# Optimization experiments

Measured on AMD Instinct MI355X. Metric: run time of the kernel, lower is better.

## Reference

```python
import jax, jax.numpy as jnp
import numpy as np

B, T, V, D, OUT = 32, 100, 10000, 128, 1000
CODE_P = 0.003  # ~30 active codes per visit


def gru_dir(x3, whh, bhh, reverse):
    """x3: [B,T,3F] precomputed input-side gates (W_ih x + b_ih). PyTorch GRU math."""
    F = whh.shape[1]
    h0 = jnp.zeros((x3.shape[0], F), x3.dtype)

    def step(h, xt):
        gh = h @ whh.T + bhh
        xr, xz, xn = jnp.split(xt, 3, -1)
        hr, hz, hn = jnp.split(gh, 3, -1)
        r = jax.nn.sigmoid(xr + hr)
        z = jax.nn.sigmoid(xz + hz)
        n = jnp.tanh(xn + r * hn)
        h_new = (1.0 - z) * n + z * h
        return h_new, h_new

    _, hs = jax.lax.scan(step, h0, jnp.swapaxes(x3, 0, 1), reverse=reverse)
    return jnp.swapaxes(hs, 0, 1)  # [B,T,F]


def setup_inputs() -> dict:
    key = jax.random.key(0)
    ks = jax.random.split(key, 16)
    s = lambda k, *sh: jax.random.normal(k, sh, dtype=jnp.float32) * 0.05
    # multi-hot visits, ~0/1 with density CODE_P; force code 0 present so no all-zero visit
    x = (jax.random.uniform(ks[0], (B, T, V)) < CODE_P).astype(jnp.float32)
    x = x.at[:, :, 0].set(1.0)
    return {
        "batchdata": x,
        "emb": s(ks[1], V, D),
        "wih_f": s(ks[2], 3 * D, D), "whh_f": s(ks[3], 3 * D, D),
        "bih_f": jnp.zeros((3 * D,), jnp.float32), "bhh_f": jnp.zeros((3 * D,), jnp.float32),
        "wih_b": s(ks[4], 3 * D, D), "whh_b": s(ks[5], 3 * D, D),
        "bih_b": jnp.zeros((3 * D,), jnp.float32), "bhh_b": jnp.zeros((3 * D,), jnp.float32),
        "attn_w": s(ks[6], 2 * D, 1), "attn_b": jnp.zeros((1,), jnp.float32),
        "comb_w": s(ks[7], D, 4 * D), "comb_b": jnp.zeros((D,), jnp.float32),
        "fc_w": s(ks[8], OUT, D), "fc_b": jnp.zeros((OUT,), jnp.float32),
    }


def reference(batchdata, emb, wih_f, whh_f, bih_f, bhh_f, wih_b, whh_b, bih_b, bhh_b,
              attn_w, attn_b, comb_w, comb_b, fc_w, fc_b):
    # multihot_to_embedding: sum of embedding rows where visit==1 == multihot @ table
    e = jnp.einsum('btv,vd->btd', batchdata, emb)          # [B,T,D]
    mask = jnp.any(e != 0, axis=2)                          # [B,T]
    # DipoleLayer: bidirectional GRU (hidden=D each dir), dropout in eval mode = identity
    xf = jnp.einsum('btf,gf->btg', e, wih_f) + bih_f
    xb = jnp.einsum('btf,gf->btg', e, wih_b) + bih_b
    hf = gru_dir(xf, whh_f, bhh_f, reverse=False)
    hb = gru_dir(xb, whh_b, bhh_b, reverse=True)
    h = jnp.concatenate([hf, hb], axis=-1)                  # [B,T,2D]
    # location-based attention over timesteps
    scores = (h @ attn_w)[..., 0] + attn_b[0]               # [B,T]
    scores = jnp.where(mask, scores, jnp.float32(-1e9))
    a = jax.nn.softmax(scores, axis=-1)
    c = jnp.einsum('bt,btf->bf', a, h)                      # [B,2D] context
    last = jnp.sum(mask.astype(jnp.int32), axis=-1) - 1     # last valid visit
    h_last = h[jnp.arange(h.shape[0]), last]                # [B,2D]
    feat = jnp.tanh(jnp.concatenate([c, h_last], -1) @ comb_w.T + comb_b)  # [B,D]
    logits = feat @ fc_w.T + fc_b                           # [B,OUT]
    return logits
```

## Files before the change

### kernel.cpp

```cpp
#include <hip/hip_runtime.h>
#include <math.h>

#define BB 32
#define TT 100
#define VV 10000
#define DD 128
#define OUTN 1000
#define G3 384

__global__ __launch_bounds__(256) void k_embed(
    const float* __restrict__ x, const float* __restrict__ emb,
    float* __restrict__ e, int* __restrict__ mask)
{
    const int bt  = blockIdx.x;
    const int tid = threadIdx.x;
    __shared__ int   s_cnt;
    __shared__ int   s_any;
    __shared__ int   s_idx[256];
    __shared__ float s_val[256];
    if (tid == 0) { s_cnt = 0; s_any = 0; }
    __syncthreads();

    const float4* x4 = (const float4*)(x + (size_t)bt * VV);
    for (int i = tid; i < VV / 4; i += 256) {
        float4 v = x4[i];
        if (v.x != 0.f) { int p = atomicAdd(&s_cnt, 1); if (p < 256) { s_idx[p] = 4*i+0; s_val[p] = v.x; } }
        if (v.y != 0.f) { int p = atomicAdd(&s_cnt, 1); if (p < 256) { s_idx[p] = 4*i+1; s_val[p] = v.y; } }
        if (v.z != 0.f) { int p = atomicAdd(&s_cnt, 1); if (p < 256) { s_idx[p] = 4*i+2; s_val[p] = v.z; } }
        if (v.w != 0.f) { int p = atomicAdd(&s_cnt, 1); if (p < 256) { s_idx[p] = 4*i+3; s_val[p] = v.w; } }
    }
    __syncthreads();
    int cnt = s_cnt; if (cnt > 256) cnt = 256;
    if (tid < DD) {
        float acc = 0.f;
        for (int i = 0; i < cnt; ++i)
            acc += s_val[i] * emb[(size_t)s_idx[i] * DD + tid];
        e[(size_t)bt * DD + tid] = acc;
        if (acc != 0.f) s_any = 1;
    }
    __syncthreads();
    if (tid == 0) mask[bt] = s_any;
}

__global__ __launch_bounds__(256) void k_gates(
    const float* __restrict__ e,
    const float* __restrict__ wih_f, const float* __restrict__ bih_f,
    const float* __restrict__ wih_b, const float* __restrict__ bih_b,
    float* __restrict__ x3)
{
    const int r0  = blockIdx.x * 8;
    const int tid = threadIdx.x;
    __shared__ __align__(16) float se[8][DD];
    for (int i = tid; i < 8 * DD; i += 256)
        se[i >> 7][i & 127] = e[(size_t)(r0 + (i >> 7)) * DD + (i & 127)];
    __syncthreads();

    for (int cc = 0; cc < 3; ++cc) {
        const int col = tid + cc * 256;
        const float* wrow;
        float bias;
        if (col < G3) { wrow = wih_f + (size_t)col * DD;        bias = bih_f[col]; }
        else          { wrow = wih_b + (size_t)(col - G3) * DD; bias = bih_b[col - G3]; }
        float acc[8];
        #pragma unroll
        for (int r = 0; r < 8; ++r) acc[r] = 0.f;
        const float4* w4 = (const float4*)wrow;
        for (int k4 = 0; k4 < DD / 4; ++k4) {
            float4 w = w4[k4];
            #pragma unroll
            for (int r = 0; r < 8; ++r) {
                float4 ev = *(const float4*)&se[r][4 * k4];
                acc[r] += ev.x * w.x + ev.y * w.y + ev.z * w.z + ev.w * w.w;
            }
        }
        #pragma unroll
        for (int r = 0; r < 8; ++r)
            x3[(size_t)(r0 + r) * 768 + col] = acc[r] + bias;
    }
}

__global__ __launch_bounds__(256, 1) void k_gru(
    const float* __restrict__ x3,
    const float* __restrict__ whh_f, const float* __restrict__ bhh_f,
    const float* __restrict__ whh_b, const float* __restrict__ bhh_b,
    float* __restrict__ h_all)
{
    const int dir = blockIdx.x & 1;
    const int b   = blockIdx.x >> 1;
    const int tid = threadIdx.x;
    const int g   = tid & 127;
    const int kh  = tid >> 7;
    const int kb  = kh * 64;
    const float* whh = dir ? whh_b : whh_f;
    const float* bhh = dir ? bhh_b : bhh_f;

    const float4* pr4 = (const float4*)(whh + (size_t)(g         ) * DD + kb);
    const float4* pz4 = (const float4*)(whh + (size_t)(DD     + g) * DD + kb);
    const float4* pn4 = (const float4*)(whh + (size_t)(2 * DD + g) * DD + kb);

#define Q16(M) M(0) M(1) M(2) M(3) M(4) M(5) M(6) M(7) M(8) M(9) M(10) M(11) M(12) M(13) M(14) M(15)
#define DECLW(i) float4 wr##i = pr4[i], wz##i = pz4[i], wn##i = pn4[i];
    Q16(DECLW)

    const float bhr = bhh[g], bhz = bhh[DD + g], bhn = bhh[2 * DD + g];

    __shared__ __align__(16) float h_lds[DD];
    __shared__ float p_lds[3 * DD];
    float h_reg = 0.f;
    if (tid < DD) h_lds[tid] = 0.f;
    __syncthreads();

    for (int t = 0; t < TT; ++t) {
        const int te = dir ? (TT - 1 - t) : t;
        const float* x3p = x3 + (size_t)(b * TT + te) * 768 + dir * G3;
        float xr = 0.f, xz = 0.f, xn = 0.f;
        if (tid < DD) { xr = x3p[g]; xz = x3p[DD + g]; xn = x3p[2 * DD + g]; }

        float ar0 = 0.f, ar1 = 0.f, az0 = 0.f, az1 = 0.f, an0 = 0.f, an1 = 0.f;
#define FMA(i) { float4 hv = *(const float4*)&h_lds[kb + 4 * (i)]; \
        (((i)&1) ? ar1 : ar0) += wr##i.x*hv.x + wr##i.y*hv.y + wr##i.z*hv.z + wr##i.w*hv.w; \
        (((i)&1) ? az1 : az0) += wz##i.x*hv.x + wz##i.y*hv.y + wz##i.z*hv.z + wz##i.w*hv.w; \
        (((i)&1) ? an1 : an0) += wn##i.x*hv.x + wn##i.y*hv.y + wn##i.z*hv.z + wn##i.w*hv.w; }
        Q16(FMA)
#undef FMA
        const float pr = ar0 + ar1, pz = az0 + az1, pn = an0 + an1;

        if (kh) { p_lds[g] = pr; p_lds[DD + g] = pz; p_lds[2 * DD + g] = pn; }
        __syncthreads();

        if (tid < DD) {
            float hr = pr + p_lds[g]          + bhr;
            float hz = pz + p_lds[DD + g]     + bhz;
            float hn = pn + p_lds[2 * DD + g] + bhn;
            float r  = __builtin_amdgcn_rcpf(1.f + __expf(-(xr + hr)));
            float z  = __builtin_amdgcn_rcpf(1.f + __expf(-(xz + hz)));
            float e2 = __expf(2.f * (xn + r * hn));
            float n  = 1.f - 2.f * __builtin_amdgcn_rcpf(e2 + 1.f);
            float hnew = n + z * (h_reg - n);
            h_reg = hnew;
            h_lds[g] = hnew;
            h_all[(size_t)((dir * BB + b) * TT + te) * DD + g] = hnew;
        }
        __syncthreads();
    }
#undef DECLW
#undef Q16
}

__global__ __launch_bounds__(256) void k_attn(
    const float* __restrict__ h_all, const int* __restrict__ mask,
    const float* __restrict__ attn_w, const float* __restrict__ attn_b,
    const float* __restrict__ comb_w, const float* __restrict__ comb_b,
    float* __restrict__ feat)
{
    const int b   = blockIdx.x;
    const int tid = threadIdx.x;
    __shared__ float s_aw[256];
    __shared__ float s_sc[128];
    __shared__ int   s_m[128];
    __shared__ float s_red[128];
    __shared__ __align__(16) float s_ch[512];

    s_aw[tid] = attn_w[tid];
    int m = 0;
    if (tid < 128) {
        m = (tid < TT) ? mask[b * TT + tid] : 0;
        s_m[tid] = m;
    }
    __syncthreads();
    for (int s = 64; s > 0; s >>= 1) {
        if (tid < s) s_m[tid] += s_m[tid + s];
        __syncthreads();
    }
    const int last = s_m[0] - 1;

    const float* hf = h_all + (size_t)(0 * BB + b) * TT * DD;
    const float* hb = h_all + (size_t)(1 * BB + b) * TT * DD;

    float sc = -1e9f;
    if (tid < TT) {
        float a = attn_b[0];
        const float4* hf4 = (const float4*)(hf + (size_t)tid * DD);
        const float4* hb4 = (const float4*)(hb + (size_t)tid * DD);
        for (int k = 0; k < DD / 4; ++k) {
            float4 v = hf4[k];
            a += v.x * s_aw[4*k] + v.y * s_aw[4*k+1] + v.z * s_aw[4*k+2] + v.w * s_aw[4*k+3];
        }
        for (int k = 0; k < DD / 4; ++k) {
            float4 v = hb4[k];
            a += v.x * s_aw[DD+4*k] + v.y * s_aw[DD+4*k+1] + v.z * s_aw[DD+4*k+2] + v.w * s_aw[DD+4*k+3];
        }
        sc = m ? a : -1e9f;
    }
    if (tid < 128) { s_sc[tid] = sc; s_red[tid] = sc; }
    __syncthreads();
    for (int s = 64; s > 0; s >>= 1) {
        if (tid < s) s_red[tid] = fmaxf(s_red[tid], s_red[tid + s]);
        __syncthreads();
    }
    const float mx = s_red[0];
    __syncthreads();
    float ex = 0.f;
    if (tid < 128) { ex = __expf(s_sc[tid] - mx); s_sc[tid] = ex; s_red[tid] = ex; }
    __syncthreads();
    for (int s = 64; s > 0; s >>= 1) {
        if (tid < s) s_red[tid] += s_red[tid + s];
        __syncthreads();
    }
    const float inv = 1.f / s_red[0];
    __syncthreads();

    {
        const int fl = tid & 127;
        const float* hp = (tid < 128) ? hf : hb;
        float csum = 0.f;
        for (int t = 0; t < TT; ++t)
            csum += s_sc[t] * hp[(size_t)t * DD + fl];
        s_ch[tid]       = csum * inv;
        s_ch[256 + tid] = hp[(size_t)last * DD + fl];
    }
    __syncthreads();

    if (tid < 128) {
        float a = comb_b[tid];
        const float4* cw = (const float4*)(comb_w + (size_t)tid * 512);
        for (int k = 0; k < 128; ++k) {
            float4 w4 = cw[k];
            float4 v4 = *(const float4*)&s_ch[4 * k];
            a += w4.x * v4.x + w4.y * v4.y + w4.z * v4.z + w4.w * v4.w;
        }
        feat[(size_t)b * DD + tid] = tanhf(a);
    }
}

__global__ __launch_bounds__(256) void k_logits(
    const float* __restrict__ feat, const float* __restrict__ fc_w,
    const float* __restrict__ fc_b, float* __restrict__ out)
{
    const int b   = blockIdx.x >> 2;
    const int oc  = blockIdx.x & 3;
    const int tid = threadIdx.x;
    const int o   = oc * 256 + tid;
    __shared__ __align__(16) float s_f[DD];
    if (tid < DD) s_f[tid] = feat[(size_t)b * DD + tid];
    __syncthreads();
    if (o < OUTN) {
        float a = fc_b[o];
        const float4* w4 = (const float4*)(fc_w + (size_t)o * DD);
        for (int k = 0; k < DD / 4; ++k) {
            float4 w = w4[k];
            float4 v = *(const float4*)&s_f[4 * k];
            a += w.x * v.x + w.y * v.y + w.z * v.z + w.w * v.w;
        }
        out[(size_t)b * OUTN + o] = a;
    }
}

extern "C" void kernel_launch(void* const* d_in, const int* in_sizes, int n_in,
                              void* d_out, int out_size, void* d_ws, size_t ws_size,
                              hipStream_t stream)
{
    const float* x      = (const float*)d_in[0];
    const float* emb    = (const float*)d_in[1];
    const float* wih_f  = (const float*)d_in[2];
    const float* whh_f  = (const float*)d_in[3];
    const float* bih_f  = (const float*)d_in[4];
    const float* bhh_f  = (const float*)d_in[5];
    const float* wih_b  = (const float*)d_in[6];
    const float* whh_b  = (const float*)d_in[7];
    const float* bih_b  = (const float*)d_in[8];
    const float* bhh_b  = (const float*)d_in[9];
    const float* attn_w = (const float*)d_in[10];
    const float* attn_b = (const float*)d_in[11];
    const float* comb_w = (const float*)d_in[12];
    const float* comb_b = (const float*)d_in[13];
    const float* fc_w   = (const float*)d_in[14];
    const float* fc_b   = (const float*)d_in[15];
    float* out = (float*)d_out;

    float* ws    = (float*)d_ws;
    float* e     = ws;
    int*   mask  = (int*)(ws + 409600);
    float* x3    = ws + 412800;
    float* h_all = ws + 2870400;
    float* feat  = ws + 3689600;

    k_embed <<<BB * TT,      256, 0, stream>>>(x, emb, e, mask);
    k_gates <<<(BB * TT)/8,  256, 0, stream>>>(e, wih_f, bih_f, wih_b, bih_b, x3);
    k_gru   <<<2 * BB,       256, 0, stream>>>(x3, whh_f, bhh_f, whh_b, bhh_b, h_all);
    k_attn  <<<BB,           256, 0, stream>>>(h_all, mask, attn_w, attn_b, comb_w, comb_b, feat);
    k_logits<<<BB * 4,       256, 0, stream>>>(feat, fc_w, fc_b, out);
}
```

Before: 372.9 us.

## Split GRU recurrent matvec across four K-quarters and prefetch next-step gate inputs

The GRU recurrence kernel now runs 512 threads per block, splitting the K dimension of the hidden matvec into four quarters instead of two. This halves the per-thread weight registers and the serial FMA chain per timestep, and partial sums are combined through a larger LDS buffer. The input-side gate values for the next timestep are loaded one iteration ahead, hiding global latency behind the current step. Empty asm statements pin the weights in VGPRs. In exchange, the reduction does more LDS reads and each barrier spans more waves.

```diff
diff --git a/kernel.cpp b/kernel.cpp
--- a/kernel.cpp
+++ b/kernel.cpp
@@ -79,7 +79,7 @@
     }
 }
 
-__global__ __launch_bounds__(256, 1) void k_gru(
+__global__ __launch_bounds__(512, 2) void k_gru(
     const float* __restrict__ x3,
     const float* __restrict__ whh_f, const float* __restrict__ bhh_f,
     const float* __restrict__ whh_b, const float* __restrict__ bhh_b,
@@ -89,8 +89,8 @@
     const int b   = blockIdx.x >> 1;
     const int tid = threadIdx.x;
     const int g   = tid & 127;
-    const int kh  = tid >> 7;
-    const int kb  = kh * 64;
+    const int kq  = tid >> 7;
+    const int kb  = kq * 32;
     const float* whh = dir ? whh_b : whh_f;
     const float* bhh = dir ? bhh_b : bhh_f;
 
@@ -98,40 +98,61 @@
     const float4* pz4 = (const float4*)(whh + (size_t)(DD     + g) * DD + kb);
     const float4* pn4 = (const float4*)(whh + (size_t)(2 * DD + g) * DD + kb);
 
-#define Q16(M) M(0) M(1) M(2) M(3) M(4) M(5) M(6) M(7) M(8) M(9) M(10) M(11) M(12) M(13) M(14) M(15)
+#define Q8(M) M(0) M(1) M(2) M(3) M(4) M(5) M(6) M(7)
 #define DECLW(i) float4 wr##i = pr4[i], wz##i = pz4[i], wn##i = pn4[i];
-    Q16(DECLW)
-
-    const float bhr = bhh[g], bhz = bhh[DD + g], bhn = bhh[2 * DD + g];
+    Q8(DECLW)
+#define KEEP(i) asm("" : "+v"(wr##i.x), "+v"(wr##i.y), "+v"(wr##i.z), "+v"(wr##i.w), \
+                         "+v"(wz##i.x), "+v"(wz##i.y), "+v"(wz##i.z), "+v"(wz##i.w), \
+                         "+v"(wn##i.x), "+v"(wn##i.y), "+v"(wn##i.z), "+v"(wn##i.w));
+    Q8(KEEP)
+#undef KEEP
+
+    float bhr = 0.f, bhz = 0.f, bhn = 0.f;
+    if (tid < DD) { bhr = bhh[g]; bhz = bhh[DD + g]; bhn = bhh[2 * DD + g]; }
 
     __shared__ __align__(16) float h_lds[DD];
-    __shared__ float p_lds[3 * DD];
+    __shared__ float p_lds[9 * DD];
     float h_reg = 0.f;
     if (tid < DD) h_lds[tid] = 0.f;
+
+    float xr = 0.f, xz = 0.f, xn = 0.f;
+    {
+        const float* x3p = x3 + (size_t)(b * TT + (dir ? TT - 1 : 0)) * 768 + dir * G3;
+        if (tid < DD) { xr = x3p[g]; xz = x3p[DD + g]; xn = x3p[2 * DD + g]; }
+    }
     __syncthreads();
 
     for (int t = 0; t < TT; ++t) {
         const int te = dir ? (TT - 1 - t) : t;
-        const float* x3p = x3 + (size_t)(b * TT + te) * 768 + dir * G3;
-        float xr = 0.f, xz = 0.f, xn = 0.f;
-        if (tid < DD) { xr = x3p[g]; xz = x3p[DD + g]; xn = x3p[2 * DD + g]; }
+
+        float nxr = 0.f, nxz = 0.f, nxn = 0.f;
+        if (t + 1 < TT) {
+            const int tn = dir ? (TT - 2 - t) : (t + 1);
+            const float* x3n = x3 + (size_t)(b * TT + tn) * 768 + dir * G3;
+            if (tid < DD) { nxr = x3n[g]; nxz = x3n[DD + g]; nxn = x3n[2 * DD + g]; }
+        }
 
         float ar0 = 0.f, ar1 = 0.f, az0 = 0.f, az1 = 0.f, an0 = 0.f, an1 = 0.f;
 #define FMA(i) { float4 hv = *(const float4*)&h_lds[kb + 4 * (i)]; \
         (((i)&1) ? ar1 : ar0) += wr##i.x*hv.x + wr##i.y*hv.y + wr##i.z*hv.z + wr##i.w*hv.w; \
         (((i)&1) ? az1 : az0) += wz##i.x*hv.x + wz##i.y*hv.y + wz##i.z*hv.z + wz##i.w*hv.w; \
         (((i)&1) ? an1 : an0) += wn##i.x*hv.x + wn##i.y*hv.y + wn##i.z*hv.z + wn##i.w*hv.w; }
-        Q16(FMA)
+        Q8(FMA)
 #undef FMA
         const float pr = ar0 + ar1, pz = az0 + az1, pn = an0 + an1;
 
-        if (kh) { p_lds[g] = pr; p_lds[DD + g] = pz; p_lds[2 * DD + g] = pn; }
+        if (kq) {
+            const int q = (kq - 1) * 3;
+            p_lds[(q + 0) * DD + g] = pr;
+            p_lds[(q + 1) * DD + g] = pz;
+            p_lds[(q + 2) * DD + g] = pn;
+        }
         __syncthreads();
 
         if (tid < DD) {
-            float hr = pr + p_lds[g]          + bhr;
-            float hz = pz + p_lds[DD + g]     + bhz;
-            float hn = pn + p_lds[2 * DD + g] + bhn;
+            float hr = pr + p_lds[0*DD+g] + p_lds[3*DD+g] + p_lds[6*DD+g] + bhr;
+            float hz = pz + p_lds[1*DD+g] + p_lds[4*DD+g] + p_lds[7*DD+g] + bhz;
+            float hn = pn + p_lds[2*DD+g] + p_lds[5*DD+g] + p_lds[8*DD+g] + bhn;
             float r  = __builtin_amdgcn_rcpf(1.f + __expf(-(xr + hr)));
             float z  = __builtin_amdgcn_rcpf(1.f + __expf(-(xz + hz)));
             float e2 = __expf(2.f * (xn + r * hn));
@@ -142,9 +163,10 @@
             h_all[(size_t)((dir * BB + b) * TT + te) * DD + g] = hnew;
         }
         __syncthreads();
+        xr = nxr; xz = nxz; xn = nxn;
     }
 #undef DECLW
-#undef Q16
+#undef Q8
 }
 
 __global__ __launch_bounds__(256) void k_attn(
@@ -287,7 +309,7 @@
 
     k_embed <<<BB * TT,      256, 0, stream>>>(x, emb, e, mask);
     k_gates <<<(BB * TT)/8,  256, 0, stream>>>(e, wih_f, bih_f, wih_b, bih_b, x3);
-    k_gru   <<<2 * BB,       256, 0, stream>>>(x3, whh_f, bhh_f, whh_b, bhh_b, h_all);
+    k_gru   <<<2 * BB,       512, 0, stream>>>(x3, whh_f, bhh_f, whh_b, bhh_b, h_all);
     k_attn  <<<BB,           256, 0, stream>>>(h_all, mask, attn_w, attn_b, comb_w, comb_b, feat);
     k_logits<<<BB * 4,       256, 0, stream>>>(feat, fc_w, fc_b, out);
 }
```

Result: faster. 351.6 us (-5.7%).
